# Performance work log

Measured on AMD Instinct MI355X. Metric: run time of the kernel, lower is better.

Reference implementation:

```python
import jax, jax.numpy as jnp
import numpy as np

LAMBDA_M = 1.0
NUM_GRU_LAYERS = 3

B, S, H, G = 64, 512, 768, 768


def setup_inputs() -> dict:
    key = jax.random.key(0)
    ks = jax.random.split(key, 12)
    std = 0.02
    # variable-length attention mask (all rows non-empty)
    lengths = jax.random.randint(ks[0], (B,), S // 4, S + 1)
    attention_mask = (jnp.arange(S)[None, :] < lengths[:, None]).astype(jnp.float32)
    return {
        "sentence_representation": jax.random.normal(ks[1], (B, H), jnp.float32),
        "attention_mask": attention_mask,
        "aspect_embedding": jax.random.normal(ks[2], (B, H), jnp.float32),
        "sentence_embeddings": jax.random.normal(ks[3], (B, S, H), jnp.float32),
        "ws": std * jax.random.normal(ks[4], (H, H), jnp.float32),
        "wa": std * jax.random.normal(ks[5], (H, H), jnp.float32),
        "w": std * jax.random.normal(ks[6], (H,), jnp.float32),
        "whs": std * jax.random.normal(ks[7], (H, G), jnp.float32),
        "wd1": std * jax.random.normal(ks[8], (H, H), jnp.float32),
        "wd": std * jax.random.normal(ks[9], (G, H), jnp.float32),
        "w_ih": std * jax.random.normal(ks[10], (3 * G, H), jnp.float32),  # GRU input weights (r,z,n)
        "w_hh": std * jax.random.normal(ks[11], (3 * G, G), jnp.float32),  # GRU hidden weights (r,z,n)
    }


def _gru_cell(x, h, w_ih, w_hh):
    # standard GRU cell, bias=False (torch gate order: r, z, n)
    gi = x @ w_ih.T  # (B, 3G)
    gh = h @ w_hh.T  # (B, 3G)
    i_r, i_z, i_n = jnp.split(gi, 3, axis=-1)
    h_r, h_z, h_n = jnp.split(gh, 3, axis=-1)
    r = jax.nn.sigmoid(i_r + h_r)
    z = jax.nn.sigmoid(i_z + h_z)
    n = jnp.tanh(i_n + r * h_n)
    return (1.0 - z) * n + z * h


def reference(sentence_representation, attention_mask, aspect_embedding,
              sentence_embeddings, ws, wa, w, whs, wd1, wd, w_ih, w_hh):
    # Hoist loop-invariant projections (same math as recomputing per layer)
    Se = jnp.einsum('bsh,hk->bsk', sentence_embeddings, ws)  # (B,S,H)
    A = aspect_embedding @ wa                                 # (B,H)
    mask = attention_mask                                     # (B,S)
    denom = mask.sum(-1, keepdims=True)                       # (B,1)
    h = sentence_representation
    for t in range(NUM_GRU_LAYERS):
        Wd = wd1 if t == 0 else wd
        M = Se + (h @ Wd)[:, None, :] + A[:, None, :]         # (B,S,H)
        scores = jnp.tanh(M) @ w                              # (B,S)
        m = jax.nn.softmax(LAMBDA_M * scores, axis=-1)        # (B,S)
        # reweighted masked-mean pooling
        at = jnp.einsum('bs,bsh->bh', m * mask, sentence_embeddings) / denom
        if t == 0:
            h = h @ whs                                       # project to GRU hidden dim
        h = _gru_cell(at, h, w_ih, w_hh)
    return h
```

## Files before the change

### kernel.cpp

```cpp
#include <hip/hip_runtime.h>
#include <hip/hip_bf16.h>
#include <stdint.h>

#define Bdim 64
#define Sdim 512
#define Hdim 768
#define G3   2304

typedef float f32x4 __attribute__((ext_vector_type(4)));
typedef short s16x8 __attribute__((ext_vector_type(8)));
typedef short s16x4 __attribute__((ext_vector_type(4)));

__device__ __forceinline__ float bf2f(unsigned short u){
  union { unsigned int i; float f; } c; c.i = ((unsigned int)u) << 16; return c.f;
}
__device__ __forceinline__ unsigned short f2bf(float f){
  union { float f; unsigned int i; } c; c.f = f;
  unsigned int x = c.i;
  return (unsigned short)((x + 0x7fffu + ((x >> 16) & 1u)) >> 16);
}
__device__ __forceinline__ float fast_tanh(float x){
  float e = __expf(2.f * x);
  return 1.f - 2.f / (e + 1.f);
}
__device__ __forceinline__ float fast_sigmoid(float x){
  return 1.f / (1.f + __expf(-x));
}
__device__ __forceinline__ void gload16(const void* g, void* l){
  __builtin_amdgcn_global_load_lds((const __attribute__((address_space(1))) void*)g,
                                   (__attribute__((address_space(3))) void*)l, 16, 0, 0);
}

__global__ __launch_bounds__(256) void k_prep(const float* __restrict__ SE, unsigned short* __restrict__ SEb,
                                              const float* __restrict__ ws_, unsigned short* __restrict__ wsbT,
                                              const float* __restrict__ wd1, unsigned short* __restrict__ wd1T,
                                              const float* __restrict__ wd,  unsigned short* __restrict__ wdT,
                                              const float* __restrict__ wa,  unsigned short* __restrict__ waT,
                                              const float* __restrict__ whs, unsigned short* __restrict__ whsT,
                                              const float* __restrict__ w_ih, unsigned short* __restrict__ w_ihb,
                                              const float* __restrict__ w_hh, unsigned short* __restrict__ w_hhb,
                                              const float* __restrict__ sr,  unsigned short* __restrict__ srb,
                                              const float* __restrict__ asp, unsigned short* __restrict__ aspb){
  __shared__ float tile[32][33];
  int bid = blockIdx.x;
  if (bid < 2880) {
    int which = bid / 576, r = bid % 576;
    const float* src; unsigned short* dst;
    switch (which) {
      case 0: src = ws_; dst = wsbT; break;
      case 1: src = wd1; dst = wd1T; break;
      case 2: src = wd;  dst = wdT;  break;
      case 3: src = wa;  dst = waT;  break;
      default: src = whs; dst = whsT; break;
    }
    int bx = (r % 24) * 32, by = (r / 24) * 32;
    int tx = threadIdx.x % 32, ty = threadIdx.x / 32;
    for (int j = ty; j < 32; j += 8) tile[j][tx] = src[(size_t)(by + j) * Hdim + bx + tx];
    __syncthreads();
    for (int j = ty; j < 32; j += 8) dst[(size_t)(bx + j) * Hdim + by + tx] = f2bf(tile[tx][j]);
    return;
  }
  bid -= 2880;
  const float* s; unsigned short* d; int j;
  if      (bid < 12288) { s = SE;   d = SEb;   j = bid * 256 + threadIdx.x; }
  else if (bid < 13152) { s = w_ih; d = w_ihb; j = (bid - 12288) * 256 + threadIdx.x; }
  else if (bid < 14016) { s = w_hh; d = w_hhb; j = (bid - 13152) * 256 + threadIdx.x; }
  else if (bid < 14040) { s = sr;   d = srb;   j = (bid - 14016) * 256 + threadIdx.x; }
  else                  { s = asp;  d = aspb;  j = (bid - 14040) * 256 + threadIdx.x; }
  const float4* sp = (const float4*)s;
  float4 a = sp[2*j], b = sp[2*j+1];
  uint4 o;
  o.x = (unsigned)f2bf(a.x) | ((unsigned)f2bf(a.y) << 16);
  o.y = (unsigned)f2bf(a.z) | ((unsigned)f2bf(a.w) << 16);
  o.z = (unsigned)f2bf(b.x) | ((unsigned)f2bf(b.y) << 16);
  o.w = (unsigned)f2bf(b.z) | ((unsigned)f2bf(b.w) << 16);
  ((uint4*)d)[j] = o;
}

__global__ __launch_bounds__(256) void k_conv_bf16(const float* __restrict__ src,
                                                   unsigned short* __restrict__ dst, int n8){
  int i = blockIdx.x * 256 + threadIdx.x;
  if (i >= n8) return;
  const float4* s = (const float4*)src;
  float4 a = s[2*i], b = s[2*i+1];
  uint4 o;
  o.x = (unsigned)f2bf(a.x) | ((unsigned)f2bf(a.y) << 16);
  o.y = (unsigned)f2bf(a.z) | ((unsigned)f2bf(a.w) << 16);
  o.z = (unsigned)f2bf(b.x) | ((unsigned)f2bf(b.y) << 16);
  o.w = (unsigned)f2bf(b.z) | ((unsigned)f2bf(b.w) << 16);
  ((uint4*)dst)[i] = o;
}

__global__ __launch_bounds__(256) void k_conv4(const float* __restrict__ s0, unsigned short* __restrict__ d0, int c0,
                                               const float* __restrict__ s1, unsigned short* __restrict__ d1, int c1,
                                               const float* __restrict__ s2, unsigned short* __restrict__ d2, int c2,
                                               const float* __restrict__ s3, unsigned short* __restrict__ d3, int c3){
  int i = blockIdx.x * 256 + threadIdx.x;
  const float* s; unsigned short* d; int j;
  if (i < c0) { s = s0; d = d0; j = i; }
  else if (i < c0 + c1) { s = s1; d = d1; j = i - c0; }
  else if (i < c0 + c1 + c2) { s = s2; d = d2; j = i - c0 - c1; }
  else if (i < c0 + c1 + c2 + c3) { s = s3; d = d3; j = i - c0 - c1 - c2; }
  else return;
  const float4* sp = (const float4*)s;
  float4 a = sp[2*j], b = sp[2*j+1];
  uint4 o;
  o.x = (unsigned)f2bf(a.x) | ((unsigned)f2bf(a.y) << 16);
  o.y = (unsigned)f2bf(a.z) | ((unsigned)f2bf(a.w) << 16);
  o.z = (unsigned)f2bf(b.x) | ((unsigned)f2bf(b.y) << 16);
  o.w = (unsigned)f2bf(b.z) | ((unsigned)f2bf(b.w) << 16);
  ((uint4*)d)[j] = o;
}

__global__ __launch_bounds__(256) void k_transpose_ws(const float* __restrict__ src,
                                                      unsigned short* __restrict__ dst){
  __shared__ float tile[32][33];
  int bx = blockIdx.x * 32, by = blockIdx.y * 32;
  int tx = threadIdx.x % 32, ty = threadIdx.x / 32;
  for (int j = ty; j < 32; j += 8) tile[j][tx] = src[(size_t)(by + j) * Hdim + bx + tx];
  __syncthreads();
  for (int j = ty; j < 32; j += 8) dst[(size_t)(bx + j) * Hdim + by + tx] = f2bf(tile[tx][j]);
}

__global__ __launch_bounds__(256) void k_transpose4(const float* __restrict__ s0, unsigned short* __restrict__ d0,
                                                    const float* __restrict__ s1, unsigned short* __restrict__ d1,
                                                    const float* __restrict__ s2, unsigned short* __restrict__ d2,
                                                    const float* __restrict__ s3, unsigned short* __restrict__ d3){
  const float* src; unsigned short* dst;
  switch (blockIdx.z) {
    case 0: src = s0; dst = d0; break;
    case 1: src = s1; dst = d1; break;
    case 2: src = s2; dst = d2; break;
    default: src = s3; dst = d3; break;
  }
  __shared__ float tile[32][33];
  int bx = blockIdx.x * 32, by = blockIdx.y * 32;
  int tx = threadIdx.x % 32, ty = threadIdx.x / 32;
  for (int j = ty; j < 32; j += 8) tile[j][tx] = src[(size_t)(by + j) * Hdim + bx + tx];
  __syncthreads();
  for (int j = ty; j < 32; j += 8) dst[(size_t)(bx + j) * Hdim + by + tx] = f2bf(tile[tx][j]);
}

__global__ __launch_bounds__(256) void k_gemm_se(const unsigned short* __restrict__ A,
                                                 const unsigned short* __restrict__ Bt,
                                                 unsigned short* __restrict__ C){
  __shared__ unsigned short As[128 * 64];
  __shared__ unsigned short Bs[128 * 64];
  const int t = threadIdx.x;
  const int lane = t & 63;
  const int w = t >> 6, wr = w >> 1, wc = w & 1;
  int bid = blockIdx.x;
  int swz = (bid & 7) * 192 + (bid >> 3);
  const int m0 = (swz / 6) * 128, n0 = (swz % 6) * 128;

  f32x4 acc[4][4];
  #pragma unroll
  for (int m = 0; m < 4; m++)
    #pragma unroll
    for (int n = 0; n < 4; n++) acc[m][n] = (f32x4){0.f, 0.f, 0.f, 0.f};

  for (int k0 = 0; k0 < Hdim; k0 += 64) {
    #pragma unroll
    for (int i = 0; i < 4; i++) {
      int L = t * 16 + i * 4096;
      int row = L >> 7;
      int offp = L & 127;
      int goff = offp ^ ((row & 7) << 4);
      int wub = __builtin_amdgcn_readfirstlane((t & 192) * 16 + i * 4096);
      gload16((const char*)A  + ((size_t)(m0 + row) * Hdim + k0) * 2 + goff, (char*)As + wub);
      gload16((const char*)Bt + ((size_t)(n0 + row) * Hdim + k0) * 2 + goff, (char*)Bs + wub);
    }
    __syncthreads();
    #pragma unroll
    for (int kk = 0; kk < 2; kk++) {
      s16x8 af[4], bfr[4];
      #pragma unroll
      for (int m = 0; m < 4; m++) {
        int row = wr * 64 + m * 16 + (lane & 15);
        int sw = (row & 7) << 4;
        int kb = kk * 64 + (lane >> 4) * 8;
        s16x4 lo = *(const s16x4*)((const char*)As + row * 128 + (kb ^ sw));
        s16x4 hi = *(const s16x4*)((const char*)As + row * 128 + ((kb + 32) ^ sw));
        af[m] = __builtin_shufflevector(lo, hi, 0, 1, 2, 3, 4, 5, 6, 7);
      }
      #pragma unroll
      for (int n = 0; n < 4; n++) {
        int row = wc * 64 + n * 16 + (lane & 15);
        int sw = (row & 7) << 4;
        int kb = kk * 64 + (lane >> 4) * 8;
        s16x4 lo = *(const s16x4*)((const char*)Bs + row * 128 + (kb ^ sw));
        s16x4 hi = *(const s16x4*)((const char*)Bs + row * 128 + ((kb + 32) ^ sw));
        bfr[n] = __builtin_shufflevector(lo, hi, 0, 1, 2, 3, 4, 5, 6, 7);
      }
      #pragma unroll
      for (int m = 0; m < 4; m++)
        #pragma unroll
        for (int n = 0; n < 4; n++)
          acc[m][n] = __builtin_amdgcn_mfma_f32_16x16x32_bf16(af[m], bfr[n], acc[m][n], 0, 0, 0);
    }
    __syncthreads();
  }
  #pragma unroll
  for (int m = 0; m < 4; m++) {
    int rowb = m0 + wr * 64 + m * 16 + (lane >> 4) * 4;
    #pragma unroll
    for (int n = 0; n < 4; n++) {
      int col = n0 + wc * 64 + n * 16 + (lane & 15);
      #pragma unroll
      for (int r = 0; r < 4; r++)
        C[(size_t)(rowb + r) * Hdim + col] = f2bf(acc[m][n][r]);
    }
  }
}

__global__ __launch_bounds__(256) void k_gemm_smallM(const unsigned short* __restrict__ A,
                                                     const unsigned short* __restrict__ Bt,
                                                     float* __restrict__ C,
                                                     unsigned short* __restrict__ Cb){
  __shared__ unsigned short As[64 * 64];
  __shared__ unsigned short Bs[128 * 64];
  const int t = threadIdx.x, lane = t & 63, w = t >> 6;
  const int n0 = blockIdx.x * 128;
  f32x4 acc[4][2];
  #pragma unroll
  for (int m = 0; m < 4; m++)
    #pragma unroll
    for (int n = 0; n < 2; n++) acc[m][n] = (f32x4){0.f, 0.f, 0.f, 0.f};

  for (int k0 = 0; k0 < Hdim; k0 += 64) {
    #pragma unroll
    for (int i = 0; i < 2; i++) {
      int L = t * 16 + i * 4096, row = L >> 7, off = L & 127;
      *(uint4*)((char*)As + row * 128 + (off ^ ((row & 7) << 4))) =
        *(const uint4*)((const char*)A + ((size_t)row * Hdim + k0) * 2 + off);
    }
    #pragma unroll
    for (int i = 0; i < 4; i++) {
      int L = t * 16 + i * 4096, row = L >> 7, off = L & 127;
      *(uint4*)((char*)Bs + row * 128 + (off ^ ((row & 7) << 4))) =
        *(const uint4*)((const char*)Bt + ((size_t)(n0 + row) * Hdim + k0) * 2 + off);
    }
    __syncthreads();
    #pragma unroll
    for (int kk = 0; kk < 2; kk++) {
      s16x8 af[4], bfr[2];
      int kb = kk * 64 + (lane >> 4) * 8;
      #pragma unroll
      for (int m = 0; m < 4; m++) {
        int row = m * 16 + (lane & 15);
        int sw = (row & 7) << 4;
        s16x4 lo = *(const s16x4*)((const char*)As + row * 128 + (kb ^ sw));
        s16x4 hi = *(const s16x4*)((const char*)As + row * 128 + ((kb + 32) ^ sw));
        af[m] = __builtin_shufflevector(lo, hi, 0, 1, 2, 3, 4, 5, 6, 7);
      }
      #pragma unroll
      for (int n = 0; n < 2; n++) {
        int row = w * 32 + n * 16 + (lane & 15);
        int sw = (row & 7) << 4;
        s16x4 lo = *(const s16x4*)((const char*)Bs + row * 128 + (kb ^ sw));
        s16x4 hi = *(const s16x4*)((const char*)Bs + row * 128 + ((kb + 32) ^ sw));
        bfr[n] = __builtin_shufflevector(lo, hi, 0, 1, 2, 3, 4, 5, 6, 7);
      }
      #pragma unroll
      for (int m = 0; m < 4; m++)
        #pragma unroll
        for (int n = 0; n < 2; n++)
          acc[m][n] = __builtin_amdgcn_mfma_f32_16x16x32_bf16(af[m], bfr[n], acc[m][n], 0, 0, 0);
    }
    __syncthreads();
  }
  #pragma unroll
  for (int m = 0; m < 4; m++) {
    int rowb = m * 16 + (lane >> 4) * 4;
    #pragma unroll
    for (int n = 0; n < 2; n++) {
      int col = n0 + w * 32 + n * 16 + (lane & 15);
      #pragma unroll
      for (int r = 0; r < 4; r++) {
        float v = acc[m][n][r];
        C[(size_t)(rowb + r) * Hdim + col] = v;
        if (Cb) Cb[(size_t)(rowb + r) * Hdim + col] = f2bf(v);
      }
    }
  }
}

__global__ __launch_bounds__(256) void k_vpart(const unsigned short* __restrict__ A1,
                                               const unsigned short* __restrict__ B1t,
                                               const unsigned short* __restrict__ A2,
                                               const unsigned short* __restrict__ B2t,
                                               float* __restrict__ Vp){
  __shared__ unsigned short As[64 * 64];
  __shared__ unsigned short Bs[128 * 64];
  const int t = threadIdx.x, lane = t & 63, w = t >> 6;
  const int n0 = blockIdx.x * 128;
  const int kc = blockIdx.y;
  f32x4 acc[4][2];
  #pragma unroll
  for (int m = 0; m < 4; m++)
    #pragma unroll
    for (int n = 0; n < 2; n++) acc[m][n] = (f32x4){0.f, 0.f, 0.f, 0.f};

  #pragma unroll
  for (int gi = 0; gi < 4; gi++) {
    int g = kc * 4 + gi;
    const unsigned short* A  = (g < 12) ? A1 : A2;
    const unsigned short* Bt = (g < 12) ? B1t : B2t;
    int k0 = (g % 12) * 64;
    #pragma unroll
    for (int i = 0; i < 2; i++) {
      int L = t * 16 + i * 4096, row = L >> 7, off = L & 127;
      *(uint4*)((char*)As + row * 128 + (off ^ ((row & 7) << 4))) =
        *(const uint4*)((const char*)A + ((size_t)row * Hdim + k0) * 2 + off);
    }
    #pragma unroll
    for (int i = 0; i < 4; i++) {
      int L = t * 16 + i * 4096, row = L >> 7, off = L & 127;
      *(uint4*)((char*)Bs + row * 128 + (off ^ ((row & 7) << 4))) =
        *(const uint4*)((const char*)Bt + ((size_t)(n0 + row) * Hdim + k0) * 2 + off);
    }
    __syncthreads();
    #pragma unroll
    for (int kk = 0; kk < 2; kk++) {
      s16x8 af[4], bfr[2];
      int kb = kk * 64 + (lane >> 4) * 8;
      #pragma unroll
      for (int m = 0; m < 4; m++) {
        int row = m * 16 + (lane & 15);
        int sw = (row & 7) << 4;
        s16x4 lo = *(const s16x4*)((const char*)As + row * 128 + (kb ^ sw));
        s16x4 hi = *(const s16x4*)((const char*)As + row * 128 + ((kb + 32) ^ sw));
        af[m] = __builtin_shufflevector(lo, hi, 0, 1, 2, 3, 4, 5, 6, 7);
      }
      #pragma unroll
      for (int n = 0; n < 2; n++) {
        int row = w * 32 + n * 16 + (lane & 15);
        int sw = (row & 7) << 4;
        s16x4 lo = *(const s16x4*)((const char*)Bs + row * 128 + (kb ^ sw));
        s16x4 hi = *(const s16x4*)((const char*)Bs + row * 128 + ((kb + 32) ^ sw));
        bfr[n] = __builtin_shufflevector(lo, hi, 0, 1, 2, 3, 4, 5, 6, 7);
      }
      #pragma unroll
      for (int m = 0; m < 4; m++)
        #pragma unroll
        for (int n = 0; n < 2; n++)
          acc[m][n] = __builtin_amdgcn_mfma_f32_16x16x32_bf16(af[m], bfr[n], acc[m][n], 0, 0, 0);
    }
    __syncthreads();
  }
  float* outp = Vp + (size_t)kc * (Bdim * Hdim);
  #pragma unroll
  for (int m = 0; m < 4; m++) {
    int rowb = m * 16 + (lane >> 4) * 4;
    #pragma unroll
    for (int n = 0; n < 2; n++) {
      int col = n0 + w * 32 + n * 16 + (lane & 15);
      #pragma unroll
      for (int r = 0; r < 4; r++)
        outp[(size_t)(rowb + r) * Hdim + col] = acc[m][n][r];
    }
  }
}

__global__ __launch_bounds__(256) void k_scores(const unsigned short* __restrict__ Seb,
                                                const float* __restrict__ Vp,
                                                const float* __restrict__ wv,
                                                float* __restrict__ scores){
  int b = blockIdx.y;
  int s_base = blockIdx.x * 16;
  int t = threadIdx.x, lane = t & 63, w = t >> 6;
  f32x4 v0 = {0,0,0,0}, v1 = {0,0,0,0}, v2 = {0,0,0,0};
  #pragma unroll
  for (int kc = 0; kc < 6; kc++) {
    const float* Vb = Vp + ((size_t)kc * Bdim + b) * Hdim;
    v0 += *(const f32x4*)(Vb + lane * 8);
    v1 += *(const f32x4*)(Vb + lane * 8 + 4);
    v2 += *(const f32x4*)(Vb + 512 + lane * 4);
  }
  f32x4 w0 = *(const f32x4*)(wv + lane * 8);
  f32x4 w1 = *(const f32x4*)(wv + lane * 8 + 4);
  f32x4 w2 = *(const f32x4*)(wv + 512 + lane * 4);
  #pragma unroll
  for (int si = 0; si < 4; si++) {
    int s = s_base + w * 4 + si;
    const unsigned short* rp = Seb + ((size_t)b * Sdim + s) * Hdim;
    ushort4 p0 = *(const ushort4*)(rp + lane * 8);
    ushort4 p1 = *(const ushort4*)(rp + lane * 8 + 4);
    ushort4 p2 = *(const ushort4*)(rp + 512 + lane * 4);
    float acc;
    acc  = fast_tanh(bf2f(p0.x) + v0[0]) * w0[0];
    acc += fast_tanh(bf2f(p0.y) + v0[1]) * w0[1];
    acc += fast_tanh(bf2f(p0.z) + v0[2]) * w0[2];
    acc += fast_tanh(bf2f(p0.w) + v0[3]) * w0[3];
    acc += fast_tanh(bf2f(p1.x) + v1[0]) * w1[0];
    acc += fast_tanh(bf2f(p1.y) + v1[1]) * w1[1];
    acc += fast_tanh(bf2f(p1.z) + v1[2]) * w1[2];
    acc += fast_tanh(bf2f(p1.w) + v1[3]) * w1[3];
    acc += fast_tanh(bf2f(p2.x) + v2[0]) * w2[0];
    acc += fast_tanh(bf2f(p2.y) + v2[1]) * w2[1];
    acc += fast_tanh(bf2f(p2.z) + v2[2]) * w2[2];
    acc += fast_tanh(bf2f(p2.w) + v2[3]) * w2[3];
    #pragma unroll
    for (int o = 32; o; o >>= 1) acc += __shfl_xor(acc, o);
    if (lane == 0) scores[(size_t)b * Sdim + s] = acc;
  }
}

__global__ __launch_bounds__(192) void k_at_sm_bf16(const unsigned short* __restrict__ SEb,
                                                    const float* __restrict__ scores,
                                                    const float* __restrict__ mask,
                                                    float* __restrict__ at_part){
  int sc = blockIdx.x, b = blockIdx.y;
  int t = threadIdx.x, lane = t & 63, w = t >> 6;
  __shared__ float sbuf[512];
  __shared__ float mbuf[512];
  __shared__ float red[3], red2[3];
  __shared__ float msh[64];
  __shared__ float half0[96 * 8];
  float lmax = -1e30f;
  #pragma unroll
  for (int j = 0; j < 3; j++) {
    int idx = t + 192 * j;
    if (idx < 512) {
      float v = scores[(size_t)b * Sdim + idx];
      float mk = mask[(size_t)b * Sdim + idx];
      sbuf[idx] = v; mbuf[idx] = mk;
      lmax = fmaxf(lmax, v);
    }
  }
  #pragma unroll
  for (int o = 32; o; o >>= 1) lmax = fmaxf(lmax, __shfl_xor(lmax, o));
  if (lane == 0) red[w] = lmax;
  __syncthreads();
  float mx = fmaxf(fmaxf(red[0], red[1]), red[2]);
  float le = 0.f, lm = 0.f;
  #pragma unroll
  for (int j = 0; j < 3; j++) {
    int idx = t + 192 * j;
    if (idx < 512) {
      float e = __expf(sbuf[idx] - mx);
      le += e; lm += mbuf[idx];
      sbuf[idx] = e * mbuf[idx];
    }
  }
  #pragma unroll
  for (int o = 32; o; o >>= 1) { le += __shfl_xor(le, o); lm += __shfl_xor(lm, o); }
  __syncthreads();
  if (lane == 0) { red[w] = le; red2[w] = lm; }
  __syncthreads();
  float inv = 1.f / ((red[0] + red[1] + red[2]) * (red2[0] + red2[1] + red2[2]));
  if (t < 64) msh[t] = sbuf[sc * 64 + t] * inv;
  __syncthreads();
  int hseg = t % 96, sh = t / 96;
  const unsigned short* base = SEb + ((size_t)b * Sdim + sc * 64 + sh * 32) * Hdim + hseg * 8;
  float acc[8] = {0, 0, 0, 0, 0, 0, 0, 0};
  for (int s = 0; s < 32; s++) {
    float m = msh[sh * 32 + s];
    ushort4 a = *(const ushort4*)(base + (size_t)s * Hdim);
    ushort4 c = *(const ushort4*)(base + (size_t)s * Hdim + 4);
    acc[0] += m * bf2f(a.x); acc[1] += m * bf2f(a.y); acc[2] += m * bf2f(a.z); acc[3] += m * bf2f(a.w);
    acc[4] += m * bf2f(c.x); acc[5] += m * bf2f(c.y); acc[6] += m * bf2f(c.z); acc[7] += m * bf2f(c.w);
  }
  if (sh == 0) {
    #pragma unroll
    for (int j = 0; j < 8; j++) half0[hseg * 8 + j] = acc[j];
  }
  __syncthreads();
  if (sh == 1) {
    float* op = at_part + ((size_t)sc * Bdim + b) * Hdim + hseg * 8;
    #pragma unroll
    for (int j = 0; j < 8; j++) op[j] = acc[j] + half0[hseg * 8 + j];
  }
}

__global__ __launch_bounds__(192) void k_at_sm_f32(const float* __restrict__ SE,
                                                   const float* __restrict__ scores,
                                                   const float* __restrict__ mask,
                                                   float* __restrict__ at_part){
  int sc = blockIdx.x, b = blockIdx.y;
  int t = threadIdx.x, lane = t & 63, w = t >> 6;
  __shared__ float sbuf[512];
  __shared__ float mbuf[512];
  __shared__ float red[3], red2[3];
  __shared__ float msh[64];
  __shared__ float half0[96 * 8];
  float lmax = -1e30f;
  #pragma unroll
  for (int j = 0; j < 3; j++) {
    int idx = t + 192 * j;
    if (idx < 512) {
      float v = scores[(size_t)b * Sdim + idx];
      float mk = mask[(size_t)b * Sdim + idx];
      sbuf[idx] = v; mbuf[idx] = mk;
      lmax = fmaxf(lmax, v);
    }
  }
  #pragma unroll
  for (int o = 32; o; o >>= 1) lmax = fmaxf(lmax, __shfl_xor(lmax, o));
  if (lane == 0) red[w] = lmax;
  __syncthreads();
  float mx = fmaxf(fmaxf(red[0], red[1]), red[2]);
  float le = 0.f, lm = 0.f;
  #pragma unroll
  for (int j = 0; j < 3; j++) {
    int idx = t + 192 * j;
    if (idx < 512) {
      float e = __expf(sbuf[idx] - mx);
      le += e; lm += mbuf[idx];
      sbuf[idx] = e * mbuf[idx];
    }
  }
  #pragma unroll
  for (int o = 32; o; o >>= 1) { le += __shfl_xor(le, o); lm += __shfl_xor(lm, o); }
  __syncthreads();
  if (lane == 0) { red[w] = le; red2[w] = lm; }
  __syncthreads();
  float inv = 1.f / ((red[0] + red[1] + red[2]) * (red2[0] + red2[1] + red2[2]));
  if (t < 64) msh[t] = sbuf[sc * 64 + t] * inv;
  __syncthreads();
  int hseg = t % 96, sh = t / 96;
  const float* base = SE + ((size_t)b * Sdim + sc * 64 + sh * 32) * Hdim + hseg * 8;
  float acc[8] = {0, 0, 0, 0, 0, 0, 0, 0};
  for (int s = 0; s < 32; s++) {
    float m = msh[sh * 32 + s];
    float4 a = *(const float4*)(base + (size_t)s * Hdim);
    float4 c = *(const float4*)(base + (size_t)s * Hdim + 4);
    acc[0] += m * a.x; acc[1] += m * a.y; acc[2] += m * a.z; acc[3] += m * a.w;
    acc[4] += m * c.x; acc[5] += m * c.y; acc[6] += m * c.z; acc[7] += m * c.w;
  }
  if (sh == 0) {
    #pragma unroll
    for (int j = 0; j < 8; j++) half0[hseg * 8 + j] = acc[j];
  }
  __syncthreads();
  if (sh == 1) {
    float* op = at_part + ((size_t)sc * Bdim + b) * Hdim + hseg * 8;
    #pragma unroll
    for (int j = 0; j < 8; j++) op[j] = acc[j] + half0[hseg * 8 + j];
  }
}

__global__ __launch_bounds__(256) void k_at_reduce(const float* __restrict__ at_part,
                                                   unsigned short* __restrict__ atb){
  int i = blockIdx.x * 256 + threadIdx.x;
  float s = 0.f;
  #pragma unroll
  for (int p = 0; p < 8; p++) s += at_part[(size_t)p * (Bdim * Hdim) + i];
  atb[i] = f2bf(s);
}

__global__ __launch_bounds__(256) void k_gates2(const unsigned short* __restrict__ atb,
                                                const unsigned short* __restrict__ hb,
                                                const unsigned short* __restrict__ w_ihb,
                                                const unsigned short* __restrict__ w_hhb,
                                                float* __restrict__ gi2,
                                                float* __restrict__ gh2){
  __shared__ unsigned short As[64 * 64];
  __shared__ unsigned short Bs[128 * 64];
  const int t = threadIdx.x, lane = t & 63, w = t >> 6;
  const int n0 = blockIdx.x * 128;
  const int z = blockIdx.y, kc = blockIdx.z;
  const unsigned short* A  = z ? hb : atb;
  const unsigned short* Bt = z ? w_hhb : w_ihb;
  float* outp = (z ? gh2 : gi2) + (size_t)kc * (Bdim * G3);
  f32x4 acc[4][2];
  #pragma unroll
  for (int m = 0; m < 4; m++)
    #pragma unroll
    for (int n = 0; n < 2; n++) acc[m][n] = (f32x4){0.f, 0.f, 0.f, 0.f};

  for (int it = 0; it < 6; it++) {
    int k0 = kc * 384 + it * 64;
    #pragma unroll
    for (int i = 0; i < 2; i++) {
      int L = t * 16 + i * 4096, row = L >> 7, off = L & 127;
      *(uint4*)((char*)As + row * 128 + (off ^ ((row & 7) << 4))) =
        *(const uint4*)((const char*)A + ((size_t)row * Hdim + k0) * 2 + off);
    }
    #pragma unroll
    for (int i = 0; i < 4; i++) {
      int L = t * 16 + i * 4096, row = L >> 7, off = L & 127;
      *(uint4*)((char*)Bs + row * 128 + (off ^ ((row & 7) << 4))) =
        *(const uint4*)((const char*)Bt + ((size_t)(n0 + row) * Hdim + k0) * 2 + off);
    }
    __syncthreads();
    #pragma unroll
    for (int kk = 0; kk < 2; kk++) {
      s16x8 af[4], bfr[2];
      int kb = kk * 64 + (lane >> 4) * 8;
      #pragma unroll
      for (int m = 0; m < 4; m++) {
        int row = m * 16 + (lane & 15);
        int sw = (row & 7) << 4;
        s16x4 lo = *(const s16x4*)((const char*)As + row * 128 + (kb ^ sw));
        s16x4 hi = *(const s16x4*)((const char*)As + row * 128 + ((kb + 32) ^ sw));
        af[m] = __builtin_shufflevector(lo, hi, 0, 1, 2, 3, 4, 5, 6, 7);
      }
      #pragma unroll
      for (int n = 0; n < 2; n++) {
        int row = w * 32 + n * 16 + (lane & 15);
        int sw = (row & 7) << 4;
        s16x4 lo = *(const s16x4*)((const char*)Bs + row * 128 + (kb ^ sw));
        s16x4 hi = *(const s16x4*)((const char*)Bs + row * 128 + ((kb + 32) ^ sw));
        bfr[n] = __builtin_shufflevector(lo, hi, 0, 1, 2, 3, 4, 5, 6, 7);
      }
      #pragma unroll
      for (int m = 0; m < 4; m++)
        #pragma unroll
        for (int n = 0; n < 2; n++)
          acc[m][n] = __builtin_amdgcn_mfma_f32_16x16x32_bf16(af[m], bfr[n], acc[m][n], 0, 0, 0);
    }
    __syncthreads();
  }
  #pragma unroll
  for (int m = 0; m < 4; m++) {
    int rowb = m * 16 + (lane >> 4) * 4;
    #pragma unroll
    for (int n = 0; n < 2; n++) {
      int col = n0 + w * 32 + n * 16 + (lane & 15);
      #pragma unroll
      for (int r = 0; r < 4; r++)
        outp[(size_t)(rowb + r) * G3 + col] = acc[m][n][r];
    }
  }
}

__global__ __launch_bounds__(256) void k_gru_elem2(const float* __restrict__ gi2,
                                                   const float* __restrict__ gh2,
                                                   const float* __restrict__ h,
                                                   float* __restrict__ hout,
                                                   unsigned short* __restrict__ hbout){
  int i = blockIdx.x * 256 + threadIdx.x;
  int b = i / Hdim, g = i % Hdim;
  const size_t P = (size_t)Bdim * G3;
  const float* gia = gi2 + (size_t)b * G3;
  const float* gha = gh2 + (size_t)b * G3;
  float ir = gia[g] + gia[P + g];
  float iz = gia[Hdim + g] + gia[P + Hdim + g];
  float in_ = gia[2 * Hdim + g] + gia[P + 2 * Hdim + g];
  float hr = gha[g] + gha[P + g];
  float hz = gha[Hdim + g] + gha[P + Hdim + g];
  float hn = gha[2 * Hdim + g] + gha[P + 2 * Hdim + g];
  float r = fast_sigmoid(ir + hr);
  float z = fast_sigmoid(iz + hz);
  float n = fast_tanh(in_ + r * hn);
  float ho = (1.f - z) * n + z * h[i];
  hout[i] = ho;
  hbout[i] = f2bf(ho);
}

extern "C" void kernel_launch(void* const* d_in, const int* in_sizes, int n_in,
                              void* d_out, int out_size, void* d_ws, size_t ws_size,
                              hipStream_t stream) {
  const float* sr   = (const float*)d_in[0];
  const float* mask = (const float*)d_in[1];
  const float* asp  = (const float*)d_in[2];
  const float* SE   = (const float*)d_in[3];
  const float* ws_  = (const float*)d_in[4];
  const float* wa   = (const float*)d_in[5];
  const float* wv   = (const float*)d_in[6];
  const float* whs  = (const float*)d_in[7];
  const float* wd1  = (const float*)d_in[8];
  const float* wd   = (const float*)d_in[9];
  const float* w_ih = (const float*)d_in[10];
  const float* w_hh = (const float*)d_in[11];
  float* out = (float*)d_out;

  char* p = (char*)d_ws;
  size_t offA = 0;
  auto A_ = [&](size_t b) -> char* { char* r = p + offA; offA += b; return r; };
  unsigned short* Seb  = (unsigned short*)A_(50331648);
  unsigned short* wsbT = (unsigned short*)A_(1179648);
  unsigned short* SEb  = (unsigned short*)A_(50331648);

  const size_t othersBytes = 18100224;
  bool keepSEb = (offA + othersBytes) <= ws_size;
  char* q = keepSEb ? (p + offA) : (char*)SEb;
  size_t o2 = 0;
  auto B_ = [&](size_t b) -> char* { char* r = q + o2; o2 += b; return r; };
  unsigned short* w_ihb = (unsigned short*)B_(3538944);
  unsigned short* w_hhb = (unsigned short*)B_(3538944);
  unsigned short* wd1T  = (unsigned short*)B_(1179648);
  unsigned short* wdT   = (unsigned short*)B_(1179648);
  unsigned short* waT   = (unsigned short*)B_(1179648);
  unsigned short* whsT  = (unsigned short*)B_(1179648);
  unsigned short* srb   = (unsigned short*)B_(98304);
  unsigned short* aspb  = (unsigned short*)B_(98304);
  float* Vp      = (float*)B_(1179648);
  float* scores  = (float*)B_(131072);
  float* at_part = (float*)B_(1572864);
  unsigned short* atb = (unsigned short*)B_(98304);
  float* gi2     = (float*)B_(1179648);
  float* gh2     = (float*)B_(1179648);
  float* hA      = (float*)B_(196608);
  float* hB      = (float*)B_(196608);
  unsigned short* hbA = (unsigned short*)B_(98304);
  unsigned short* hbB = (unsigned short*)B_(98304);
  if (!keepSEb && (offA > ws_size)) return;

  if (keepSEb) {
    k_prep<<<dim3(16944), dim3(256), 0, stream>>>(SE, SEb, ws_, wsbT, wd1, wd1T, wd, wdT,
                                                  wa, waT, whs, whsT, w_ih, w_ihb, w_hh, w_hhb,
                                                  sr, srb, asp, aspb);
    k_gemm_se<<<dim3(1536), dim3(256), 0, stream>>>(SEb, wsbT, Seb);
  } else {
    k_conv_bf16<<<dim3(12288), dim3(256), 0, stream>>>(SE, SEb, 3145728);
    k_transpose_ws<<<dim3(24, 24), dim3(256), 0, stream>>>(ws_, wsbT);
    k_gemm_se<<<dim3(1536), dim3(256), 0, stream>>>(SEb, wsbT, Seb);
    k_transpose4<<<dim3(24, 24, 4), dim3(256), 0, stream>>>(wd1, wd1T, wd, wdT, wa, waT, whs, whsT);
    k_conv4<<<dim3(1776), dim3(256), 0, stream>>>(w_ih, w_ihb, 221184, w_hh, w_hhb, 221184,
                                                  sr, srb, 6144, asp, aspb, 6144);
  }
  k_gemm_smallM<<<dim3(6), dim3(256), 0, stream>>>(srb, whsT, hA, hbA);
  k_vpart<<<dim3(6, 6), dim3(256), 0, stream>>>(srb, wd1T, aspb, waT, Vp);

  const float* hcur = hA;
  const unsigned short* hbcur = hbA;
  for (int tl = 0; tl < 3; ++tl) {
    if (tl > 0)
      k_vpart<<<dim3(6, 6), dim3(256), 0, stream>>>(hbcur, wdT, aspb, waT, Vp);
    k_scores<<<dim3(32, 64), dim3(256), 0, stream>>>(Seb, Vp, wv, scores);
    if (keepSEb)
      k_at_sm_bf16<<<dim3(8, 64), dim3(192), 0, stream>>>(SEb, scores, mask, at_part);
    else
      k_at_sm_f32<<<dim3(8, 64), dim3(192), 0, stream>>>(SE, scores, mask, at_part);
    k_at_reduce<<<dim3(192), dim3(256), 0, stream>>>(at_part, atb);
    k_gates2<<<dim3(18, 2, 2), dim3(256), 0, stream>>>(atb, hbcur, w_ihb, w_hhb, gi2, gh2);
    float* hout = (tl == 2) ? out : ((hcur == hA) ? hB : hA);
    unsigned short* hbout = (hbcur == hbA) ? hbB : hbA;
    k_gru_elem2<<<dim3(192), dim3(256), 0, stream>>>(gi2, gh2, hcur, hout, hbout);
    hcur = hout;
    hbcur = hbout;
  }
}
```

Baseline: 241.9 us.

## Fuse at-partial reduction into gates GEMM and merge init GEMMs into one launch

Removes the separate k_at_reduce kernel: the gates GEMM now sums the 8 fp32 partials and converts to bf16 while filling its A tile in shared memory. It also merges the initial hidden projection and the first V-part GEMM into a single launch with an extra grid row, and adds an occupancy hint of 3 blocks per CU to the Se GEMM. The aim is fewer kernel launches and less global traffic per GRU layer. In exchange, each gates block (18 per kc slice) reads all 8 partials redundantly, and the occupancy hint may force register spills.

New measurement: 310.9 us. 28.5% more time.

```diff
diff --git a/kernel.cpp b/kernel.cpp
--- a/kernel.cpp
+++ b/kernel.cpp
@@ -141,9 +141,9 @@
   for (int j = ty; j < 32; j += 8) dst[(size_t)(bx + j) * Hdim + by + tx] = f2bf(tile[tx][j]);
 }
 
-__global__ __launch_bounds__(256) void k_gemm_se(const unsigned short* __restrict__ A,
-                                                 const unsigned short* __restrict__ Bt,
-                                                 unsigned short* __restrict__ C){
+__global__ __launch_bounds__(256, 3) void k_gemm_se(const unsigned short* __restrict__ A,
+                                                    const unsigned short* __restrict__ Bt,
+                                                    unsigned short* __restrict__ C){
   __shared__ unsigned short As[128 * 64];
   __shared__ unsigned short Bs[128 * 64];
   const int t = threadIdx.x;
@@ -213,14 +213,13 @@
   }
 }
 
-__global__ __launch_bounds__(256) void k_gemm_smallM(const unsigned short* __restrict__ A,
-                                                     const unsigned short* __restrict__ Bt,
-                                                     float* __restrict__ C,
-                                                     unsigned short* __restrict__ Cb){
-  __shared__ unsigned short As[64 * 64];
-  __shared__ unsigned short Bs[128 * 64];
+__device__ __forceinline__ void smallM_body(const unsigned short* __restrict__ A,
+                                            const unsigned short* __restrict__ Bt,
+                                            float* __restrict__ C, unsigned short* __restrict__ Cb,
+                                            char* ldsbuf, int n0){
+  unsigned short* As = (unsigned short*)ldsbuf;
+  unsigned short* Bs = (unsigned short*)(ldsbuf + 8192);
   const int t = threadIdx.x, lane = t & 63, w = t >> 6;
-  const int n0 = blockIdx.x * 128;
   f32x4 acc[4][2];
   #pragma unroll
   for (int m = 0; m < 4; m++)
@@ -285,16 +284,15 @@
   }
 }
 
-__global__ __launch_bounds__(256) void k_vpart(const unsigned short* __restrict__ A1,
-                                               const unsigned short* __restrict__ B1t,
-                                               const unsigned short* __restrict__ A2,
-                                               const unsigned short* __restrict__ B2t,
-                                               float* __restrict__ Vp){
-  __shared__ unsigned short As[64 * 64];
-  __shared__ unsigned short Bs[128 * 64];
+__device__ __forceinline__ void vpart_body(const unsigned short* __restrict__ A1,
+                                           const unsigned short* __restrict__ B1t,
+                                           const unsigned short* __restrict__ A2,
+                                           const unsigned short* __restrict__ B2t,
+                                           float* __restrict__ Vp,
+                                           char* ldsbuf, int n0, int kc){
+  unsigned short* As = (unsigned short*)ldsbuf;
+  unsigned short* Bs = (unsigned short*)(ldsbuf + 8192);
   const int t = threadIdx.x, lane = t & 63, w = t >> 6;
-  const int n0 = blockIdx.x * 128;
-  const int kc = blockIdx.y;
   f32x4 acc[4][2];
   #pragma unroll
   for (int m = 0; m < 4; m++)
@@ -360,6 +358,27 @@
         outp[(size_t)(rowb + r) * Hdim + col] = acc[m][n][r];
     }
   }
+}
+
+__global__ __launch_bounds__(256) void k_vpart(const unsigned short* __restrict__ A1,
+                                               const unsigned short* __restrict__ B1t,
+                                               const unsigned short* __restrict__ A2,
+                                               const unsigned short* __restrict__ B2t,
+                                               float* __restrict__ Vp){
+  __shared__ char lds[24576];
+  vpart_body(A1, B1t, A2, B2t, Vp, lds, blockIdx.x * 128, blockIdx.y);
+}
+
+__global__ __launch_bounds__(256) void k_init2(const unsigned short* __restrict__ srb,
+                                               const unsigned short* __restrict__ whsT,
+                                               float* __restrict__ hA, unsigned short* __restrict__ hbA,
+                                               const unsigned short* __restrict__ wd1T,
+                                               const unsigned short* __restrict__ aspb,
+                                               const unsigned short* __restrict__ waT,
+                                               float* __restrict__ Vp){
+  __shared__ char lds[24576];
+  if (blockIdx.y == 6) smallM_body(srb, whsT, hA, hbA, lds, blockIdx.x * 128);
+  else                 vpart_body(srb, wd1T, aspb, waT, Vp, lds, blockIdx.x * 128, blockIdx.y);
 }
 
 __global__ __launch_bounds__(256) void k_scores(const unsigned short* __restrict__ Seb,
@@ -540,16 +559,7 @@
   }
 }
 
-__global__ __launch_bounds__(256) void k_at_reduce(const float* __restrict__ at_part,
-                                                   unsigned short* __restrict__ atb){
-  int i = blockIdx.x * 256 + threadIdx.x;
-  float s = 0.f;
-  #pragma unroll
-  for (int p = 0; p < 8; p++) s += at_part[(size_t)p * (Bdim * Hdim) + i];
-  atb[i] = f2bf(s);
-}
-
-__global__ __launch_bounds__(256) void k_gates2(const unsigned short* __restrict__ atb,
+__global__ __launch_bounds__(256) void k_gates2(const float* __restrict__ at_part,
                                                 const unsigned short* __restrict__ hb,
                                                 const unsigned short* __restrict__ w_ihb,
                                                 const unsigned short* __restrict__ w_hhb,
@@ -560,7 +570,6 @@
   const int t = threadIdx.x, lane = t & 63, w = t >> 6;
   const int n0 = blockIdx.x * 128;
   const int z = blockIdx.y, kc = blockIdx.z;
-  const unsigned short* A  = z ? hb : atb;
   const unsigned short* Bt = z ? w_hhb : w_ihb;
   float* outp = (z ? gh2 : gi2) + (size_t)kc * (Bdim * G3);
   f32x4 acc[4][2];
@@ -571,11 +580,36 @@
 
   for (int it = 0; it < 6; it++) {
     int k0 = kc * 384 + it * 64;
-    #pragma unroll
-    for (int i = 0; i < 2; i++) {
-      int L = t * 16 + i * 4096, row = L >> 7, off = L & 127;
-      *(uint4*)((char*)As + row * 128 + (off ^ ((row & 7) << 4))) =
-        *(const uint4*)((const char*)A + ((size_t)row * Hdim + k0) * 2 + off);
+    if (z == 0) {
+      #pragma unroll
+      for (int i = 0; i < 2; i++) {
+        int L = t * 16 + i * 4096, row = L >> 7, off = L & 127;
+        int e0 = off >> 1;
+        const float* ap = at_part + (size_t)row * Hdim + k0 + e0;
+        float4 sa = *(const float4*)(ap);
+        float4 sb = *(const float4*)(ap + 4);
+        #pragma unroll
+        for (int pp = 1; pp < 8; pp++) {
+          const float* aq = ap + (size_t)pp * (Bdim * Hdim);
+          float4 ta = *(const float4*)(aq);
+          float4 tb = *(const float4*)(aq + 4);
+          sa.x += ta.x; sa.y += ta.y; sa.z += ta.z; sa.w += ta.w;
+          sb.x += tb.x; sb.y += tb.y; sb.z += tb.z; sb.w += tb.w;
+        }
+        uint4 o;
+        o.x = (unsigned)f2bf(sa.x) | ((unsigned)f2bf(sa.y) << 16);
+        o.y = (unsigned)f2bf(sa.z) | ((unsigned)f2bf(sa.w) << 16);
+        o.z = (unsigned)f2bf(sb.x) | ((unsigned)f2bf(sb.y) << 16);
+        o.w = (unsigned)f2bf(sb.z) | ((unsigned)f2bf(sb.w) << 16);
+        *(uint4*)((char*)As + row * 128 + (off ^ ((row & 7) << 4))) = o;
+      }
+    } else {
+      #pragma unroll
+      for (int i = 0; i < 2; i++) {
+        int L = t * 16 + i * 4096, row = L >> 7, off = L & 127;
+        *(uint4*)((char*)As + row * 128 + (off ^ ((row & 7) << 4))) =
+          *(const uint4*)((const char*)hb + ((size_t)row * Hdim + k0) * 2 + off);
+      }
     }
     #pragma unroll
     for (int i = 0; i < 4; i++) {
@@ -696,6 +730,7 @@
   float* hB      = (float*)B_(196608);
   unsigned short* hbA = (unsigned short*)B_(98304);
   unsigned short* hbB = (unsigned short*)B_(98304);
+  (void)atb;
   if (!keepSEb && (offA > ws_size)) return;
 
   if (keepSEb) {
@@ -711,8 +746,7 @@
     k_conv4<<<dim3(1776), dim3(256), 0, stream>>>(w_ih, w_ihb, 221184, w_hh, w_hhb, 221184,
                                                   sr, srb, 6144, asp, aspb, 6144);
   }
-  k_gemm_smallM<<<dim3(6), dim3(256), 0, stream>>>(srb, whsT, hA, hbA);
-  k_vpart<<<dim3(6, 6), dim3(256), 0, stream>>>(srb, wd1T, aspb, waT, Vp);
+  k_init2<<<dim3(6, 7), dim3(256), 0, stream>>>(srb, whsT, hA, hbA, wd1T, aspb, waT, Vp);
 
   const float* hcur = hA;
   const unsigned short* hbcur = hbA;
@@ -724,8 +758,7 @@
       k_at_sm_bf16<<<dim3(8, 64), dim3(192), 0, stream>>>(SEb, scores, mask, at_part);
     else
       k_at_sm_f32<<<dim3(8, 64), dim3(192), 0, stream>>>(SE, scores, mask, at_part);
-    k_at_reduce<<<dim3(192), dim3(256), 0, stream>>>(at_part, atb);
-    k_gates2<<<dim3(18, 2, 2), dim3(256), 0, stream>>>(atb, hbcur, w_ihb, w_hhb, gi2, gh2);
+    k_gates2<<<dim3(18, 2, 2), dim3(256), 0, stream>>>(at_part, hbcur, w_ihb, w_hhb, gi2, gh2);
     float* hout = (tl == 2) ? out : ((hcur == hA) ? hB : hA);
     unsigned short* hbout = (hbcur == hbA) ? hbB : hbA;
     k_gru_elem2<<<dim3(192), dim3(256), 0, stream>>>(gi2, gh2, hcur, hout, hbout);
```
